# Performance work log

Hardware: AMD Instinct MI355X
Metric: run time of the kernel (lower is better)

The kernel has to match this reference:

```python
import jax, jax.numpy as jnp
import numpy as np

IN_FEATURES = 2048
OUT_FEATURES = 2048
BATCH = 4096


def setup_inputs() -> dict:
    key = jax.random.key(0)
    k1, k2, k3, k4 = jax.random.split(key, 4)
    bound = 1.0 / (IN_FEATURES ** 0.5)
    x_re = jax.random.normal(k1, (BATCH, IN_FEATURES), dtype=jnp.float32)
    x_im = jax.random.normal(k2, (BATCH, IN_FEATURES), dtype=jnp.float32)
    # filters: (out_features, in_features), re/im each uniform(-bound, bound)
    w_re = jax.random.uniform(k3, (OUT_FEATURES, IN_FEATURES), dtype=jnp.float32, minval=-bound, maxval=bound)
    w_im = jax.random.uniform(k4, (OUT_FEATURES, IN_FEATURES), dtype=jnp.float32, minval=-bound, maxval=bound)
    return {"x_re": x_re, "x_im": x_im, "w_re": w_re, "w_im": w_im}


def reference(x_re, x_im, w_re, w_im):
    # Complex linear: (x_re + i x_im) @ (w_re + i w_im)^T, expressed as 4 real GEMMs.
    # Equivalent to torch: (inputs.unsqueeze(1) * filters).sum(-1) with complex64.
    out_re = jnp.einsum('bi,oi->bo', x_re, w_re) - jnp.einsum('bi,oi->bo', x_im, w_im)
    out_im = jnp.einsum('bi,oi->bo', x_re, w_im) + jnp.einsum('bi,oi->bo', x_im, w_re)
    # stack re/im -> (2, batch, out) to keep a single real-dtype output
    return jnp.stack([out_re, out_im], axis=0)
```

## Files before the change

kernel.cpp:

```cpp
#include <hip/hip_runtime.h>

typedef __bf16 bf16_t;
typedef __bf16 bf16x8 __attribute__((ext_vector_type(8)));
typedef __bf16 bf16x4 __attribute__((ext_vector_type(4)));
typedef float f32x4 __attribute__((ext_vector_type(4)));

#define M_DIM 4096
#define N_DIM 4096
#define K_DIM 4096
#define OUTF 2048
#define INF 2048
#define LDK 4096
#define NT 64

__global__ __launch_bounds__(256) void pack_ab(
    const float* __restrict__ xre, const float* __restrict__ xim,
    const float* __restrict__ wre, const float* __restrict__ wim,
    bf16_t* __restrict__ Abf, bf16_t* __restrict__ Bbf)
{
  size_t gid = (size_t)blockIdx.x * 256 + threadIdx.x;
  size_t e8  = gid * 8;
  const size_t MAT = (size_t)4096 * 4096;
  bool isB = e8 >= MAT;
  size_t e = isB ? (e8 - MAT) : e8;
  int row = (int)(e >> 12);
  int k   = (int)(e & 4095);

  const float* src;
  float s = 1.0f;
  if (!isB) {
    src = (k < INF) ? (xre + (size_t)row * INF + k)
                    : (xim + (size_t)row * INF + (k - INF));
  } else {
    if (row < OUTF) {
      if (k < INF) { src = wre + (size_t)row * INF + k; }
      else         { src = wim + (size_t)row * INF + (k - INF); s = -1.0f; }
    } else {
      int o = row - OUTF;
      src = (k < INF) ? (wim + (size_t)o * INF + k)
                      : (wre + (size_t)o * INF + (k - INF));
    }
  }
  const float4* p = reinterpret_cast<const float4*>(src);
  float4 f0 = p[0];
  float4 f1 = p[1];
  bf16x8 v;
  v[0] = (bf16_t)(f0.x * s); v[1] = (bf16_t)(f0.y * s);
  v[2] = (bf16_t)(f0.z * s); v[3] = (bf16_t)(f0.w * s);
  v[4] = (bf16_t)(f1.x * s); v[5] = (bf16_t)(f1.y * s);
  v[6] = (bf16_t)(f1.z * s); v[7] = (bf16_t)(f1.w * s);
  bf16_t* dst = (isB ? Bbf : Abf) + e;
  *reinterpret_cast<bf16x8*>(dst) = v;
}

__device__ __forceinline__ void gld_lds16(const void* g, void* l) {
  __builtin_amdgcn_global_load_lds(
      (const __attribute__((address_space(1))) void*)g,
      (__attribute__((address_space(3))) void*)l,
      16, 0, 0);
}


template<int QM, int QN>
__device__ __forceinline__ void mfma_quad(f32x4 (&acc)[8][4],
                                          const bf16x8 (&aF)[4][2],
                                          const bf16x8 (&bF)[2][2]) {
  __builtin_amdgcn_s_setprio(1);
#pragma unroll
  for (int m = 0; m < 4; ++m)
#pragma unroll
    for (int n = 0; n < 2; ++n) {
      f32x4 v = acc[QM * 4 + m][QN * 2 + n];
      v = __builtin_amdgcn_mfma_f32_16x16x32_bf16(aF[m][0], bF[n][0], v, 0, 0, 0);
      v = __builtin_amdgcn_mfma_f32_16x16x32_bf16(aF[m][1], bF[n][1], v, 0, 0, 0);
      acc[QM * 4 + m][QN * 2 + n] = v;
    }
  __builtin_amdgcn_s_setprio(0);
}

__global__ __launch_bounds__(512, 2) void gemm256(
    const bf16_t* __restrict__ A, const bf16_t* __restrict__ B,
    float* __restrict__ out)
{
  __shared__ alignas(16) bf16_t lds[2 * 32768];
  char* Lb = (char*)lds;

  const int tid  = threadIdx.x;
  const int lane = tid & 63;
  const int wid  = tid >> 6;
  const int wm   = wid >> 2;
  const int wn   = wid & 3;
  const int lr   = lane & 15;
  const int kg   = (lane >> 4) * 16;
  const int xm   = ((lr & 3) << 4) | (((lr >> 2) & 1) << 6);

  int bid = blockIdx.x;
  int swz = (bid & 7) * 32 + (bid >> 3);
  const int bm = swz >> 4;
  const int bn = swz & 15;

  int rS[2], kS[2];
#pragma unroll
  for (int j = 0; j < 2; ++j) {
    int P   = j * 8192 + tid * 16;
    int row = P >> 7;
    int p   = P & 127;
    int L   = p ^ ((row & 3) << 4) ^ (((row >> 2) & 1) << 6);
    rS[j] = row;
    kS[j] = L >> 1;
  }
  const bf16_t* As0 = A + (size_t)(bm * 256 + rS[0]) * LDK + kS[0];
  const bf16_t* As1 = A + (size_t)(bm * 256 + rS[1]) * LDK + kS[1];
  const bf16_t* Bs0 = B + (size_t)(bn * 256 + rS[0]) * LDK + kS[0];
  const bf16_t* Bs1 = B + (size_t)(bn * 256 + rS[1]) * LDK + kS[1];
  const int dst16 = tid * 16;

#define STAGE_A(t, h, c) do {                                                  \
    gld_lds16(As0 + (size_t)(h) * 128 * LDK + (t) * 64,                        \
              Lb + (c) * 65536 + (h) * 16384 + dst16);                         \
    gld_lds16(As1 + (size_t)(h) * 128 * LDK + (t) * 64,                        \
              Lb + (c) * 65536 + (h) * 16384 + 8192 + dst16);                  \
  } while (0)
#define STAGE_B(t, h, c) do {                                                  \
    gld_lds16(Bs0 + (size_t)(h) * 128 * LDK + (t) * 64,                        \
              Lb + (c) * 65536 + 32768 + (h) * 16384 + dst16);                 \
    gld_lds16(Bs1 + (size_t)(h) * 128 * LDK + (t) * 64,                        \
              Lb + (c) * 65536 + 32768 + (h) * 16384 + 8192 + dst16);          \
  } while (0)
#define RD_A(c, qm, m, ks)                                                     \
  (*(const bf16x8*)(Lb + (c) * 65536 + wm * 16384 +                            \
                    ((qm) * 64 + (m) * 16 + lr) * 128 +                        \
                    ((((ks) * 64) | kg) ^ xm)))
#define RD_B(c, qn, n, ks)                                                     \
  (*(const bf16x8*)(Lb + (c) * 65536 + 32768 + (wn >> 1) * 16384 +             \
                    ((wn & 1) * 64 + (qn) * 32 + (n) * 16 + lr) * 128 +        \
                    ((((ks) * 64) | kg) ^ xm)))
#define BAR()   __builtin_amdgcn_s_barrier()
#define SB()    __builtin_amdgcn_sched_barrier(0)

  f32x4 acc[8][4];
#pragma unroll
  for (int i = 0; i < 8; ++i)
#pragma unroll
    for (int j = 0; j < 4; ++j)
      acc[i][j] = (f32x4){0.f, 0.f, 0.f, 0.f};

  STAGE_A(0, 0, 0); STAGE_A(0, 1, 0);
  STAGE_B(0, 0, 0); STAGE_B(0, 1, 0);
  STAGE_A(1, 0, 1); STAGE_A(1, 1, 1);
  STAGE_B(1, 0, 1); STAGE_B(1, 1, 1);
  asm volatile("s_waitcnt vmcnt(8)" ::: "memory");
  BAR();

  for (int t = 0; t < NT; ++t) {
    const int c = t & 1;
    bf16x8 a0[4][2], a1[4][2], b0[2][2], b1[2][2];

#pragma unroll
    for (int m = 0; m < 4; ++m) {
      a0[m][0] = RD_A(c, 0, m, 0);
      a0[m][1] = RD_A(c, 0, m, 1);
    }
#pragma unroll
    for (int n = 0; n < 2; ++n) {
      b0[n][0] = RD_B(c, 0, n, 0);
      b0[n][1] = RD_B(c, 0, n, 1);
    }
    SB();
#pragma unroll
    for (int n = 0; n < 2; ++n) {
      b1[n][0] = RD_B(c, 1, n, 0);
      b1[n][1] = RD_B(c, 1, n, 1);
    }
    SB();
#pragma unroll
    for (int m = 0; m < 4; ++m) {
      a1[m][0] = RD_A(c, 1, m, 0);
      a1[m][1] = RD_A(c, 1, m, 1);
    }
    SB();

    asm volatile("s_waitcnt lgkmcnt(12)" ::: "memory");
    SB();
    mfma_quad<0, 0>(acc, a0, b0);

    asm volatile("s_waitcnt lgkmcnt(8)" ::: "memory");
    SB();
    mfma_quad<0, 1>(acc, a0, b1);

    asm volatile("s_waitcnt lgkmcnt(0)" ::: "memory");
    SB();
    BAR();

    if (t + 2 < NT) {
      STAGE_B(t + 2, 0, c); STAGE_B(t + 2, 1, c);
      STAGE_A(t + 2, 0, c); STAGE_A(t + 2, 1, c);
    }
    SB();
    mfma_quad<1, 1>(acc, a1, b1);
    mfma_quad<1, 0>(acc, a1, b0);

    if (t + 2 < NT) {
      asm volatile("s_waitcnt vmcnt(8)" ::: "memory");
    } else if (t + 1 < NT) {
      asm volatile("s_waitcnt vmcnt(0)" ::: "memory");
    }
    BAR();
  }

  const size_t imOff = (size_t)M_DIM * OUTF;
  const int fq = (lane >> 4) * 4;
  const bool isIm = (bn * 256) >= OUTF;
  float* obase = out + (isIm ? imOff : 0);
  const int colBase = bn * 256 - (isIm ? OUTF : 0) + wn * 64;
#pragma unroll
  for (int ar = 0; ar < 8; ++ar) {
    int gr = bm * 256 + wm * 128 + ar * 16 + fq;
#pragma unroll
    for (int cc = 0; cc < 4; ++cc) {
      int gc = colBase + cc * 16 + lr;
#pragma unroll
      for (int j = 0; j < 4; ++j)
        obase[(size_t)(gr + j) * OUTF + gc] = acc[ar][cc][j];
    }
  }
#undef STAGE_A
#undef STAGE_B
#undef RD_A
#undef RD_B
#undef BAR
#undef SB
}

__global__ __launch_bounds__(256) void gemm_fused(
    const float* __restrict__ xre, const float* __restrict__ xim,
    const float* __restrict__ wre, const float* __restrict__ wim,
    float* __restrict__ out)
{
  __shared__ alignas(16) bf16_t As[128 * 40];
  __shared__ alignas(16) bf16_t Bs[128 * 40];

  int tid = threadIdx.x;
  int bid = blockIdx.x;
  int swz = (bid & 7) * 128 + (bid >> 3);
  int bm = swz >> 5;
  int bn = swz & 31;

  int lane = tid & 63;
  int w    = tid >> 6;
  int wm   = (w >> 1) * 64;
  int wn   = (w & 1) * 64;
  int lr   = lane & 15;
  int lk   = (lane >> 4) * 8;

  f32x4 acc[4][4];
#pragma unroll
  for (int m = 0; m < 4; ++m)
#pragma unroll
    for (int n = 0; n < 4; ++n)
      acc[m][n] = (f32x4){0.f, 0.f, 0.f, 0.f};

  int srow = tid >> 3;
  int scol = (tid & 7) * 4;

  bool nIm  = (bn * 128) >= OUTF;
  int nbase = nIm ? (bn * 128 - OUTF) : (bn * 128);

  for (int kt = 0; kt < K_DIM / 32; ++kt) {
    int k0 = kt * 32;
    bool kHi = (k0 >= INF);
    int kk = kHi ? (k0 - INF) : k0;

    const float* Asrc = (kHi ? xim : xre) + (size_t)(bm * 128) * INF + kk;
    const float* Bsrc;
    float s = 1.0f;
    if (!nIm) { if (!kHi) { Bsrc = wre; } else { Bsrc = wim; s = -1.0f; } }
    else      { Bsrc = kHi ? wre : wim; }
    Bsrc += (size_t)nbase * INF + kk;

    float4 av[4], bv[4];
#pragma unroll
    for (int i = 0; i < 4; ++i) {
      av[i] = *reinterpret_cast<const float4*>(Asrc + (size_t)(srow + i * 32) * INF + scol);
      bv[i] = *reinterpret_cast<const float4*>(Bsrc + (size_t)(srow + i * 32) * INF + scol);
    }
    __syncthreads();
#pragma unroll
    for (int i = 0; i < 4; ++i) {
      bf16x4 a4, b4;
      a4[0] = (bf16_t)av[i].x; a4[1] = (bf16_t)av[i].y;
      a4[2] = (bf16_t)av[i].z; a4[3] = (bf16_t)av[i].w;
      b4[0] = (bf16_t)(bv[i].x * s); b4[1] = (bf16_t)(bv[i].y * s);
      b4[2] = (bf16_t)(bv[i].z * s); b4[3] = (bf16_t)(bv[i].w * s);
      *reinterpret_cast<bf16x4*>(&As[(srow + i * 32) * 40 + scol]) = a4;
      *reinterpret_cast<bf16x4*>(&Bs[(srow + i * 32) * 40 + scol]) = b4;
    }
    __syncthreads();

    bf16x8 a[4], b[4];
#pragma unroll
    for (int m = 0; m < 4; ++m)
      a[m] = *reinterpret_cast<const bf16x8*>(&As[(wm + m * 16 + lr) * 40 + lk]);
#pragma unroll
    for (int n = 0; n < 4; ++n)
      b[n] = *reinterpret_cast<const bf16x8*>(&Bs[(wn + n * 16 + lr) * 40 + lk]);
#pragma unroll
    for (int m = 0; m < 4; ++m)
#pragma unroll
      for (int n = 0; n < 4; ++n)
        acc[m][n] = __builtin_amdgcn_mfma_f32_16x16x32_bf16(a[m], b[n], acc[m][n], 0, 0, 0);
  }
  __syncthreads();

  const size_t imOff = (size_t)M_DIM * OUTF;
  int fq = (lane >> 4) * 4;
#pragma unroll
  for (int m = 0; m < 4; ++m) {
    int gr = bm * 128 + wm + m * 16 + fq;
#pragma unroll
    for (int n = 0; n < 4; ++n) {
      int gc = bn * 128 + wn + n * 16 + lr;
      float* dst = (gc < OUTF) ? (out + (size_t)gr * OUTF + gc)
                               : (out + imOff + (size_t)gr * OUTF + (gc - OUTF));
#pragma unroll
      for (int j = 0; j < 4; ++j)
        dst[(size_t)j * OUTF] = acc[m][n][j];
    }
  }
}

extern "C" void kernel_launch(void* const* d_in, const int* in_sizes, int n_in,
                              void* d_out, int out_size, void* d_ws, size_t ws_size,
                              hipStream_t stream) {
  const float* xre = (const float*)d_in[0];
  const float* xim = (const float*)d_in[1];
  const float* wre = (const float*)d_in[2];
  const float* wim = (const float*)d_in[3];
  float* out = (float*)d_out;

  const size_t need = (size_t)2 * 4096 * 4096 * sizeof(bf16_t);
  if (ws_size >= need) {
    bf16_t* Abf = (bf16_t*)d_ws;
    bf16_t* Bbf = Abf + (size_t)4096 * 4096;
    hipLaunchKernelGGL(pack_ab, dim3(16384), dim3(256), 0, stream,
                       xre, xim, wre, wim, Abf, Bbf);
    hipLaunchKernelGGL(gemm256, dim3(256), dim3(512), 0, stream,
                       Abf, Bbf, out);
  } else {
    hipLaunchKernelGGL(gemm_fused, dim3(1024), dim3(256), 0, stream,
                       xre, xim, wre, wim, out);
  }
}
```

Measured before the change: 145.1 us.

## Load GEMM B fragments directly into registers, bypassing LDS, with XCD-aware tile mapping

The B operand is no longer staged through shared memory. Each wave loads its own B fragments from global memory straight into registers, prefetching one K-step ahead. The LDS footprint is halved, A staging moves from a two-stage lookahead to a one-stage lookahead interleaved with the MFMA quads, and the block-to-tile mapping changes so each XCD covers two column tiles across all row tiles. This aims to cut LDS traffic and barrier overhead, but it adds uncoalesced, row-strided global loads, duplicated B reads across waves that share the same column, and a shallower prefetch distance.

Result: slower. 196.8 us (+35.6%).

```diff
diff --git a/kernel.cpp b/kernel.cpp
--- a/kernel.cpp
+++ b/kernel.cpp
@@ -78,11 +78,11 @@
   __builtin_amdgcn_s_setprio(0);
 }
 
-__global__ __launch_bounds__(512, 2) void gemm256(
+__global__ __launch_bounds__(512, 2) void gemm256_bd(
     const bf16_t* __restrict__ A, const bf16_t* __restrict__ B,
     float* __restrict__ out)
 {
-  __shared__ alignas(16) bf16_t lds[2 * 32768];
+  __shared__ alignas(16) bf16_t lds[2 * 16384];
   char* Lb = (char*)lds;
 
   const int tid  = threadIdx.x;
@@ -96,8 +96,10 @@
 
   int bid = blockIdx.x;
   int swz = (bid & 7) * 32 + (bid >> 3);
-  const int bm = swz >> 4;
-  const int bn = swz & 15;
+  const int xcd = swz >> 5;
+  const int cI  = swz & 31;
+  const int bm  = cI & 15;
+  const int bn  = xcd * 2 + (cI >> 4);
 
   int rS[2], kS[2];
 #pragma unroll
@@ -111,30 +113,28 @@
   }
   const bf16_t* As0 = A + (size_t)(bm * 256 + rS[0]) * LDK + kS[0];
   const bf16_t* As1 = A + (size_t)(bm * 256 + rS[1]) * LDK + kS[1];
-  const bf16_t* Bs0 = B + (size_t)(bn * 256 + rS[0]) * LDK + kS[0];
-  const bf16_t* Bs1 = B + (size_t)(bn * 256 + rS[1]) * LDK + kS[1];
   const int dst16 = tid * 16;
+
+  const bf16_t* bp[2][2];
+#pragma unroll
+  for (int qn = 0; qn < 2; ++qn)
+#pragma unroll
+    for (int n = 0; n < 2; ++n)
+      bp[qn][n] = B + (size_t)(bn * 256 + wn * 64 + qn * 32 + n * 16 + lr) * LDK
+                    + (lane >> 4) * 8;
 
 #define STAGE_A(t, h, c) do {                                                  \
     gld_lds16(As0 + (size_t)(h) * 128 * LDK + (t) * 64,                        \
-              Lb + (c) * 65536 + (h) * 16384 + dst16);                         \
+              Lb + (c) * 32768 + (h) * 16384 + dst16);                         \
     gld_lds16(As1 + (size_t)(h) * 128 * LDK + (t) * 64,                        \
-              Lb + (c) * 65536 + (h) * 16384 + 8192 + dst16);                  \
-  } while (0)
-#define STAGE_B(t, h, c) do {                                                  \
-    gld_lds16(Bs0 + (size_t)(h) * 128 * LDK + (t) * 64,                        \
-              Lb + (c) * 65536 + 32768 + (h) * 16384 + dst16);                 \
-    gld_lds16(Bs1 + (size_t)(h) * 128 * LDK + (t) * 64,                        \
-              Lb + (c) * 65536 + 32768 + (h) * 16384 + 8192 + dst16);          \
+              Lb + (c) * 32768 + (h) * 16384 + 8192 + dst16);                  \
   } while (0)
 #define RD_A(c, qm, m, ks)                                                     \
-  (*(const bf16x8*)(Lb + (c) * 65536 + wm * 16384 +                            \
+  (*(const bf16x8*)(Lb + (c) * 32768 + wm * 16384 +                            \
                     ((qm) * 64 + (m) * 16 + lr) * 128 +                        \
                     ((((ks) * 64) | kg) ^ xm)))
-#define RD_B(c, qn, n, ks)                                                     \
-  (*(const bf16x8*)(Lb + (c) * 65536 + 32768 + (wn >> 1) * 16384 +             \
-                    ((wn & 1) * 64 + (qn) * 32 + (n) * 16 + lr) * 128 +        \
-                    ((((ks) * 64) | kg) ^ xm)))
+#define LDB(qn, n, ks, t)                                                      \
+  (*(const bf16x8*)(bp[qn][n] + (size_t)(t) * 64 + (ks) * 32))
 #define BAR()   __builtin_amdgcn_s_barrier()
 #define SB()    __builtin_amdgcn_sched_barrier(0)
 
@@ -145,16 +145,23 @@
     for (int j = 0; j < 4; ++j)
       acc[i][j] = (f32x4){0.f, 0.f, 0.f, 0.f};
 
+  bf16x8 b0[2][2], b1[2][2];
+
   STAGE_A(0, 0, 0); STAGE_A(0, 1, 0);
-  STAGE_B(0, 0, 0); STAGE_B(0, 1, 0);
-  STAGE_A(1, 0, 1); STAGE_A(1, 1, 1);
-  STAGE_B(1, 0, 1); STAGE_B(1, 1, 1);
+  SB();
+#pragma unroll
+  for (int n = 0; n < 2; ++n)
+#pragma unroll
+    for (int ks = 0; ks < 2; ++ks) {
+      b0[n][ks] = LDB(0, n, ks, 0);
+      b1[n][ks] = LDB(1, n, ks, 0);
+    }
   asm volatile("s_waitcnt vmcnt(8)" ::: "memory");
-  BAR();
+  BAR(); SB();
 
   for (int t = 0; t < NT; ++t) {
     const int c = t & 1;
-    bf16x8 a0[4][2], a1[4][2], b0[2][2], b1[2][2];
+    bf16x8 a0[4][2], a1[4][2];
 
 #pragma unroll
     for (int m = 0; m < 4; ++m) {
@@ -162,50 +169,38 @@
       a0[m][1] = RD_A(c, 0, m, 1);
     }
 #pragma unroll
-    for (int n = 0; n < 2; ++n) {
-      b0[n][0] = RD_B(c, 0, n, 0);
-      b0[n][1] = RD_B(c, 0, n, 1);
-    }
-    SB();
-#pragma unroll
-    for (int n = 0; n < 2; ++n) {
-      b1[n][0] = RD_B(c, 1, n, 0);
-      b1[n][1] = RD_B(c, 1, n, 1);
-    }
-    SB();
-#pragma unroll
     for (int m = 0; m < 4; ++m) {
       a1[m][0] = RD_A(c, 1, m, 0);
       a1[m][1] = RD_A(c, 1, m, 1);
     }
+    if (t + 1 < NT) STAGE_A(t + 1, 0, c ^ 1);
+    mfma_quad<0, 0>(acc, a0, b0);
     SB();
 
-    asm volatile("s_waitcnt lgkmcnt(12)" ::: "memory");
+    if (t + 1 < NT) STAGE_A(t + 1, 1, c ^ 1);
+    mfma_quad<1, 0>(acc, a1, b0);
     SB();
-    mfma_quad<0, 0>(acc, a0, b0);
-
-    asm volatile("s_waitcnt lgkmcnt(8)" ::: "memory");
+
+    if (t + 1 < NT) {
+#pragma unroll
+      for (int n = 0; n < 2; ++n)
+#pragma unroll
+        for (int ks = 0; ks < 2; ++ks)
+          b0[n][ks] = LDB(0, n, ks, t + 1);
+    }
+    mfma_quad<1, 1>(acc, a1, b1);
     SB();
+
     mfma_quad<0, 1>(acc, a0, b1);
-
-    asm volatile("s_waitcnt lgkmcnt(0)" ::: "memory");
-    SB();
-    BAR();
-
-    if (t + 2 < NT) {
-      STAGE_B(t + 2, 0, c); STAGE_B(t + 2, 1, c);
-      STAGE_A(t + 2, 0, c); STAGE_A(t + 2, 1, c);
-    }
-    SB();
-    mfma_quad<1, 1>(acc, a1, b1);
-    mfma_quad<1, 0>(acc, a1, b0);
-
-    if (t + 2 < NT) {
+    if (t + 1 < NT) {
+#pragma unroll
+      for (int n = 0; n < 2; ++n)
+#pragma unroll
+        for (int ks = 0; ks < 2; ++ks)
+          b1[n][ks] = LDB(1, n, ks, t + 1);
       asm volatile("s_waitcnt vmcnt(8)" ::: "memory");
-    } else if (t + 1 < NT) {
-      asm volatile("s_waitcnt vmcnt(0)" ::: "memory");
-    }
-    BAR();
+    }
+    BAR(); SB();
   }
 
   const size_t imOff = (size_t)M_DIM * OUTF;
@@ -225,9 +220,8 @@
     }
   }
 #undef STAGE_A
-#undef STAGE_B
 #undef RD_A
-#undef RD_B
+#undef LDB
 #undef BAR
 #undef SB
 }
@@ -344,7 +338,7 @@
     bf16_t* Bbf = Abf + (size_t)4096 * 4096;
     hipLaunchKernelGGL(pack_ab, dim3(16384), dim3(256), 0, stream,
                        xre, xim, wre, wim, Abf, Bbf);
-    hipLaunchKernelGGL(gemm256, dim3(256), dim3(512), 0, stream,
+    hipLaunchKernelGGL(gemm256_bd, dim3(256), dim3(512), 0, stream,
                        Abf, Bbf, out);
   } else {
     hipLaunchKernelGGL(gemm_fused, dim3(1024), dim3(256), 0, stream,
```
